# Optimization experiments

Measured on AMD Instinct MI355X. Metric: run time of the kernel, lower is better.

The kernel has to match this reference:

```python
import jax, jax.numpy as jnp
import numpy as np
from jax import lax


def setup_inputs() -> dict:
    key = jax.random.key(0)
    k1, k2, k3, k4 = jax.random.split(key, 4)
    B, C, H, W = 4, 1024, 64, 64
    OUT = 2048
    refer_feat = jax.random.normal(k1, (B, C, H, W), jnp.float32)
    sup_feat = jax.random.normal(k2, (B, C, H, W), jnp.float32)
    # al_conv_one: Conv2d(2048 -> 2, k=3, pad=1); small init keeps offsets in a sane range
    w_off = jax.random.normal(k3, (2, 2 * C, 3, 3), jnp.float32) * 0.01
    b_off = jnp.zeros((2,), jnp.float32)
    # defConv1: DeformConv2d(1024 -> 2048, k=1, bias=False); weight is effectively [O, C]
    w_def = jax.random.normal(k4, (OUT, C), jnp.float32) * (1.0 / np.sqrt(C))
    return {"refer_feat": refer_feat, "sup_feat": sup_feat,
            "w_off": w_off, "b_off": b_off, "w_def": w_def}


def _deform_sample(feat, dy, dx):
    """Bilinear-sample feat[b,:, h+dy, w+dx] with zero padding outside. -> [B,C,H*W]"""
    B, C, H, W = feat.shape
    py = dy + jnp.arange(H, dtype=feat.dtype)[None, :, None]   # [B,H,W]
    px = dx + jnp.arange(W, dtype=feat.dtype)[None, None, :]   # [B,H,W]
    y0 = jnp.floor(py)
    x0 = jnp.floor(px)
    wy1 = py - y0   # frac weights
    wx1 = px - x0
    y0i = y0.astype(jnp.int32)
    x0i = x0.astype(jnp.int32)
    feat_flat = feat.reshape(B, C, H * W)

    def corner(yi, xi, wgt):
        valid = (yi >= 0) & (yi < H) & (xi >= 0) & (xi < W)
        idx = (jnp.clip(yi, 0, H - 1) * W + jnp.clip(xi, 0, W - 1)).reshape(B, 1, H * W)
        g = jnp.take_along_axis(feat_flat, idx, axis=2)          # [B,C,HW]
        return g * (wgt * valid.astype(feat.dtype)).reshape(B, 1, H * W)

    return (corner(y0i, x0i, (1 - wy1) * (1 - wx1))
            + corner(y0i, x0i + 1, (1 - wy1) * wx1)
            + corner(y0i + 1, x0i, wy1 * (1 - wx1))
            + corner(y0i + 1, x0i + 1, wy1 * wx1))


def reference(refer_feat, sup_feat, w_off, b_off, w_def):
    B, C, H, W = sup_feat.shape
    concat_feat = jnp.concatenate([refer_feat, sup_feat], axis=1)      # [B,2C,H,W]
    offset = lax.conv_general_dilated(
        concat_feat, w_off, window_strides=(1, 1), padding='SAME',
        dimension_numbers=('NCHW', 'OIHW', 'NCHW')) + b_off[None, :, None, None]  # [B,2,H,W]
    # torchvision DeformConv2d offset layout for k=1: channel 0 = dy, channel 1 = dx
    sampled = _deform_sample(sup_feat, offset[:, 0], offset[:, 1])     # [B,C,HW]
    out = jnp.einsum('oc,bcl->bol', w_def, sampled)                    # 1x1 conv as GEMM
    return out.reshape(B, w_def.shape[0], H, W)
```

## Files before the change

kernel.cpp:

```cpp
#include <hip/hip_runtime.h>

#define CC   1024
#define C2   2048
#define HH   64
#define WW   64
#define HW   4096
#define MOUT 2048
#define NB   4

typedef short  short8  __attribute__((ext_vector_type(8)));
typedef float  floatx4 __attribute__((ext_vector_type(4)));

static __device__ __forceinline__ unsigned short f2bf(float f) {
  unsigned int u = __builtin_bit_cast(unsigned int, f);
  u = u + 0x7FFFu + ((u >> 16) & 1u);
  return (unsigned short)(u >> 16);
}

static __device__ __forceinline__ void glds16(const unsigned short* g, unsigned short* l) {
  __builtin_amdgcn_global_load_lds(
      (const __attribute__((address_space(1))) void*)g,
      (__attribute__((address_space(3))) void*)l, 16, 0, 0);
}

__global__ __launch_bounds__(256)
void conv_off(const float* __restrict__ refer, const float* __restrict__ sup,
              const float* __restrict__ woff, float* __restrict__ off)
{
  const int cz = blockIdx.x;
  const int ry = blockIdx.y;
  const int b  = blockIdx.z;
  const int wv = threadIdx.x >> 6;
  const int w  = threadIdx.x & 63;
  const int h0 = ry * 8 + wv * 2;

  const int cc0 = cz * 32;
  const float* basep = (cz < 32)
      ? refer + ((size_t)b * CC + cc0) * HW
      : sup   + ((size_t)b * CC + (cc0 - CC)) * HW;

  const int gy0 = h0 - 1;
  const bool top_ok = (gy0 >= 0);
  const bool bot_ok = (h0 + 2 < HH);

  float a00 = 0.f, a01 = 0.f, a10 = 0.f, a11 = 0.f;

  float rn[4];
#pragma unroll
  for (int j = 0; j < 4; j++) {
    const bool ok = (j == 0) ? top_ok : (j == 3) ? bot_ok : true;
    rn[j] = ok ? basep[(gy0 + j) * WW + w] : 0.f;
  }

  for (int ci = 0; ci < 32; ci++) {
    float rc[4];
#pragma unroll
    for (int j = 0; j < 4; j++) rc[j] = rn[j];

    if (ci < 31) {
      const float* pn = basep + (size_t)(ci + 1) * HW;
#pragma unroll
      for (int j = 0; j < 4; j++) {
        const bool ok = (j == 0) ? top_ok : (j == 3) ? bot_ok : true;
        rn[j] = ok ? pn[(gy0 + j) * WW + w] : 0.f;
      }
    }

    float lft[4], rgt[4];
#pragma unroll
    for (int j = 0; j < 4; j++) {
      const float tl = __shfl(rc[j], (w - 1) & 63, 64);
      const float tr = __shfl(rc[j], (w + 1) & 63, 64);
      lft[j] = (w == 0)  ? 0.f : tl;
      rgt[j] = (w == 63) ? 0.f : tr;
    }

    const int cc = cc0 + ci;
    const float* wp0 = woff + (size_t)cc * 9;
    const float* wp1 = woff + (size_t)(C2 + cc) * 9;
#pragma unroll
    for (int ky = 0; ky < 3; ky++) {
      const float w00 = wp0[ky * 3 + 0], w01 = wp0[ky * 3 + 1], w02 = wp0[ky * 3 + 2];
      const float w10 = wp1[ky * 3 + 0], w11 = wp1[ky * 3 + 1], w12 = wp1[ky * 3 + 2];
      a00 += lft[ky]     * w00 + rc[ky]     * w01 + rgt[ky]     * w02;
      a01 += lft[ky]     * w10 + rc[ky]     * w11 + rgt[ky]     * w12;
      a10 += lft[ky + 1] * w00 + rc[ky + 1] * w01 + rgt[ky + 1] * w02;
      a11 += lft[ky + 1] * w10 + rc[ky + 1] * w11 + rgt[ky + 1] * w12;
    }
  }

  atomicAdd(&off[((b * 2 + 0) * HH + h0) * WW + w],     a00);
  atomicAdd(&off[((b * 2 + 1) * HH + h0) * WW + w],     a01);
  atomicAdd(&off[((b * 2 + 0) * HH + h0 + 1) * WW + w], a10);
  atomicAdd(&off[((b * 2 + 1) * HH + h0 + 1) * WW + w], a11);
}

__global__ __launch_bounds__(256)
void cvt_bf16(const float* __restrict__ src, unsigned short* __restrict__ dst, int n4)
{
  const int i = blockIdx.x * 256 + threadIdx.x;
  if (i < n4) {
    const float4 f = ((const float4*)src)[i];
    ushort4 u;
    u.x = f2bf(f.x); u.y = f2bf(f.y); u.z = f2bf(f.z); u.w = f2bf(f.w);
    ((ushort4*)dst)[i] = u;
  }
}

__global__ __launch_bounds__(256)
void sample_kern(const float* __restrict__ sup, const float* __restrict__ off,
                 const float* __restrict__ boff, unsigned short* __restrict__ St)
{
  const int h   = blockIdx.x;
  const int ct  = blockIdx.y;
  const int b   = blockIdx.z;
  const int tid = threadIdx.x;

  __shared__ float swy[64], swx[64];
  __shared__ int   sy0[64], sx0[64];
  __shared__ unsigned short tile[64 * 68];

  if (tid < 64) {
    const float dy = off[((b * 2 + 0) * HH + h) * WW + tid] + boff[0];
    const float dx = off[((b * 2 + 1) * HH + h) * WW + tid] + boff[1];
    const float py = dy + (float)h;
    const float px = dx + (float)tid;
    const float y0f = floorf(py), x0f = floorf(px);
    sy0[tid] = (int)y0f;  sx0[tid] = (int)x0f;
    swy[tid] = py - y0f;  swx[tid] = px - x0f;
  }
  __syncthreads();

  const int l   = tid & 63;
  const int cs0 = tid >> 6;
  const int y0 = sy0[l], x0 = sx0[l];
  const int y1 = y0 + 1, x1 = x0 + 1;
  const float wy1 = swy[l], wx1 = swx[l];
  const float wy0 = 1.f - wy1, wx0 = 1.f - wx1;
  const float vy0 = (y0 >= 0 && y0 < HH) ? 1.f : 0.f;
  const float vy1 = (y1 >= 0 && y1 < HH) ? 1.f : 0.f;
  const float vx0 = (x0 >= 0 && x0 < WW) ? 1.f : 0.f;
  const float vx1 = (x1 >= 0 && x1 < WW) ? 1.f : 0.f;
  const int cy0 = min(max(y0, 0), HH - 1), cy1 = min(max(y1, 0), HH - 1);
  const int cx0 = min(max(x0, 0), WW - 1), cx1 = min(max(x1, 0), WW - 1);
  const int i00 = cy0 * WW + cx0, i01 = cy0 * WW + cx1;
  const int i10 = cy1 * WW + cx0, i11 = cy1 * WW + cx1;
  const float w00 = wy0 * wx0 * vy0 * vx0;
  const float w01 = wy0 * wx1 * vy0 * vx1;
  const float w10 = wy1 * wx0 * vy1 * vx0;
  const float w11 = wy1 * wx1 * vy1 * vx1;

  const int cb = ct * 64;
  for (int cs = cs0; cs < 64; cs += 4) {
    const float* sp = sup + ((size_t)b * CC + cb + cs) * HW;
    const float v = w00 * sp[i00] + w01 * sp[i01] + w10 * sp[i10] + w11 * sp[i11];
    tile[cs * 68 + l] = f2bf(v);
  }
  __syncthreads();
  const int cq  = tid & 15;
  const int ls0 = tid >> 4;
  unsigned short* stb = St + ((size_t)b * HW + h * 64) * CC;
  for (int ls = ls0; ls < 64; ls += 16) {
    ushort4 pk;
    pk.x = tile[(cq * 4 + 0) * 68 + ls];
    pk.y = tile[(cq * 4 + 1) * 68 + ls];
    pk.z = tile[(cq * 4 + 2) * 68 + ls];
    pk.w = tile[(cq * 4 + 3) * 68 + ls];
    *(ushort4*)&stb[(size_t)ls * CC + cb + cq * 4] = pk;
  }
}

__global__ __launch_bounds__(256)
void gemm_bt(const unsigned short* __restrict__ A,
             const unsigned short* __restrict__ Bt,
             float* __restrict__ C)
{
  const int bb = blockIdx.z;
  const int n0 = blockIdx.x * 128;
  const int m0 = blockIdx.y * 128;
  const unsigned short* Bb = Bt + (size_t)bb * HW * CC;
  float* Cb = C + (size_t)bb * (size_t)MOUT * HW;

  __shared__ __align__(16) unsigned short lA[128 * 64];
  __shared__ __align__(16) unsigned short lB[128 * 64];

  const int tid  = threadIdx.x;
  const int wave = tid >> 6;
  const int lane = tid & 63;
  const int wm   = (wave >> 1) * 64;
  const int wn   = (wave & 1) * 64;
  const int lrow = lane & 15;
  const int quad = lane >> 4;

  const int g8 = lane >> 3;
  const int s8 = (lane & 7) ^ g8;
  const unsigned short* gA = A  + (size_t)(m0 + wave * 32 + g8) * CC + s8 * 8;
  const unsigned short* gB = Bb + (size_t)(n0 + wave * 32 + g8) * CC + s8 * 8;

  floatx4 acc[4][4];
#pragma unroll
  for (int i = 0; i < 4; i++)
#pragma unroll
    for (int j = 0; j < 4; j++)
      acc[i][j] = (floatx4){0.f, 0.f, 0.f, 0.f};

  for (int k0 = 0; k0 < CC; k0 += 64) {
    __syncthreads();
#pragma unroll
    for (int q = 0; q < 4; q++) {
      glds16(gA + (size_t)q * 8 * CC + k0, &lA[(wave * 32 + q * 8) * 64]);
      glds16(gB + (size_t)q * 8 * CC + k0, &lB[(wave * 32 + q * 8) * 64]);
    }
    __syncthreads();

#pragma unroll
    for (int ks = 0; ks < 2; ks++) {
      short8 af[4], bfr[4];
#pragma unroll
      for (int t = 0; t < 4; t++) {
        const int sw = ((ks * 4 + quad) ^ (lrow & 7)) * 8;
        af[t]  = *(const short8*)&lA[(wm + t * 16 + lrow) * 64 + sw];
        bfr[t] = *(const short8*)&lB[(wn + t * 16 + lrow) * 64 + sw];
      }
#pragma unroll
      for (int i = 0; i < 4; i++)
#pragma unroll
        for (int j = 0; j < 4; j++)
          acc[i][j] = __builtin_amdgcn_mfma_f32_16x16x32_bf16(af[i], bfr[j], acc[i][j], 0, 0, 0);
    }
  }

#pragma unroll
  for (int i = 0; i < 4; i++) {
    const int mbase = m0 + wm + i * 16 + quad * 4;
#pragma unroll
    for (int j = 0; j < 4; j++) {
      const int n = n0 + wn + j * 16 + lrow;
      float* cp = Cb + (size_t)mbase * HW + n;
#pragma unroll
      for (int r = 0; r < 4; r++)
        cp[(size_t)r * HW] = acc[i][j][r];
    }
  }
}

extern "C" void kernel_launch(void* const* d_in, const int* in_sizes, int n_in,
                              void* d_out, int out_size, void* d_ws, size_t ws_size,
                              hipStream_t stream)
{
  const float* refer = (const float*)d_in[0];
  const float* sup   = (const float*)d_in[1];
  const float* woff  = (const float*)d_in[2];
  const float* boff  = (const float*)d_in[3];
  const float* wdef  = (const float*)d_in[4];
  float* out = (float*)d_out;

  char* ws = (char*)d_ws;
  float* off            = (float*)ws;
  unsigned short* wdefb = (unsigned short*)(ws + (512u << 10));
  unsigned short* St    = (unsigned short*)(ws + (512u << 10) + (4u << 20));

  hipMemsetAsync(off, 0, (size_t)NB * 2 * HW * sizeof(float), stream);
  conv_off<<<dim3(64, 8, NB), 256, 0, stream>>>(refer, sup, woff, off);
  cvt_bf16<<<dim3((MOUT * CC / 4 + 255) / 256), 256, 0, stream>>>(wdef, wdefb, MOUT * CC / 4);
  sample_kern<<<dim3(HH, 16, NB), 256, 0, stream>>>(sup, off, boff, St);
  gemm_bt<<<dim3(HW / 128, MOUT / 128, NB), 256, 0, stream>>>(wdefb, St, out);
}
```

Before: 381.0 us.

## Rewrite GEMM with 256x256 tiles and triple-buffered async LDS pipeline

Replaces the 128x128 single-buffered bf16 MFMA GEMM with a 256x256 tile kernel using 512 threads. It adds a three-stage LDS ring that issues global-to-LDS loads two K-steps ahead, overlapping loads with MFMA work. It also splits each K-step into two MFMA half-phases with barriers and s_setprio. The larger tile aims to raise arithmetic intensity and hide memory latency, at the cost of more registers, more LDS and fewer blocks (512 total).

After: 387.7 us. No clear change (+1.8%).

```diff
diff --git a/kernel.cpp b/kernel.cpp
--- a/kernel.cpp
+++ b/kernel.cpp
@@ -170,72 +170,112 @@
   }
 }
 
-__global__ __launch_bounds__(256)
-void gemm_bt(const unsigned short* __restrict__ A,
-             const unsigned short* __restrict__ Bt,
-             float* __restrict__ C)
+#define STAGE_A(s, kk) do { \
+  glds16(gA + (kk),                    &lA[s][(wave * 16) * 32]); \
+  glds16(gA + (size_t)128 * CC + (kk), &lA[s][(128 + wave * 16) * 32]); \
+} while (0)
+#define STAGE_B(s, kk) do { \
+  glds16(gB + (kk),                    &lB[s][(wave * 16) * 32]); \
+  glds16(gB + (size_t)128 * CC + (kk), &lB[s][(128 + wave * 16) * 32]); \
+} while (0)
+
+__global__ __launch_bounds__(512, 2)
+void gemm_bt256(const unsigned short* __restrict__ A,
+                const unsigned short* __restrict__ Bt,
+                float* __restrict__ C)
 {
   const int bb = blockIdx.z;
-  const int n0 = blockIdx.x * 128;
-  const int m0 = blockIdx.y * 128;
+  const int n0 = blockIdx.x * 256;
+  const int m0 = blockIdx.y * 256;
   const unsigned short* Bb = Bt + (size_t)bb * HW * CC;
   float* Cb = C + (size_t)bb * (size_t)MOUT * HW;
 
-  __shared__ __align__(16) unsigned short lA[128 * 64];
-  __shared__ __align__(16) unsigned short lB[128 * 64];
+  __shared__ __align__(16) unsigned short lA[3][256 * 32];
+  __shared__ __align__(16) unsigned short lB[3][256 * 32];
 
   const int tid  = threadIdx.x;
   const int wave = tid >> 6;
   const int lane = tid & 63;
-  const int wm   = (wave >> 1) * 64;
-  const int wn   = (wave & 1) * 64;
+  const int wmA  = (wave >> 2) * 128;
+  const int wnB  = (wave & 3) * 64;
   const int lrow = lane & 15;
   const int quad = lane >> 4;
-
-  const int g8 = lane >> 3;
-  const int s8 = (lane & 7) ^ g8;
-  const unsigned short* gA = A  + (size_t)(m0 + wave * 32 + g8) * CC + s8 * 8;
-  const unsigned short* gB = Bb + (size_t)(n0 + wave * 32 + g8) * CC + s8 * 8;
-
-  floatx4 acc[4][4];
-#pragma unroll
-  for (int i = 0; i < 4; i++)
+  const int rdo  = ((quad ^ ((lrow >> 1) & 3)) << 3);
+
+  const int srow = tid >> 2;
+  const int schk = (tid & 3) ^ ((tid >> 3) & 3);
+  const unsigned short* gA = A  + (size_t)(m0 + srow) * CC + schk * 8;
+  const unsigned short* gB = Bb + (size_t)(n0 + srow) * CC + schk * 8;
+
+  STAGE_A(0, 0);  STAGE_B(0, 0);
+  STAGE_A(1, 32); STAGE_B(1, 32);
+
+  floatx4 acc[8][4];
+#pragma unroll
+  for (int i = 0; i < 8; i++)
 #pragma unroll
     for (int j = 0; j < 4; j++)
       acc[i][j] = (floatx4){0.f, 0.f, 0.f, 0.f};
 
-  for (int k0 = 0; k0 < CC; k0 += 64) {
-    __syncthreads();
-#pragma unroll
-    for (int q = 0; q < 4; q++) {
-      glds16(gA + (size_t)q * 8 * CC + k0, &lA[(wave * 32 + q * 8) * 64]);
-      glds16(gB + (size_t)q * 8 * CC + k0, &lB[(wave * 32 + q * 8) * 64]);
-    }
-    __syncthreads();
-
-#pragma unroll
-    for (int ks = 0; ks < 2; ks++) {
-      short8 af[4], bfr[4];
-#pragma unroll
-      for (int t = 0; t < 4; t++) {
-        const int sw = ((ks * 4 + quad) ^ (lrow & 7)) * 8;
-        af[t]  = *(const short8*)&lA[(wm + t * 16 + lrow) * 64 + sw];
-        bfr[t] = *(const short8*)&lB[(wn + t * 16 + lrow) * 64 + sw];
-      }
-#pragma unroll
-      for (int i = 0; i < 4; i++)
-#pragma unroll
-        for (int j = 0; j < 4; j++)
-          acc[i][j] = __builtin_amdgcn_mfma_f32_16x16x32_bf16(af[i], bfr[j], acc[i][j], 0, 0, 0);
-    }
-  }
-
-#pragma unroll
-  for (int i = 0; i < 4; i++) {
-    const int mbase = m0 + wm + i * 16 + quad * 4;
+  asm volatile("s_waitcnt vmcnt(4)" ::: "memory");
+  __builtin_amdgcn_s_barrier();
+  asm volatile("" ::: "memory");
+
+  auto tile_step = [&](int t, int cb, int sb, bool st, int vm) {
+    const int k2 = (t + 2) * 32;
+
+    short8 af[4], bfr[4];
+#pragma unroll
+    for (int i = 0; i < 4; i++)
+      af[i] = *(const short8*)&lA[cb][(wmA + i * 16 + lrow) * 32 + rdo];
+#pragma unroll
+    for (int j = 0; j < 4; j++)
+      bfr[j] = *(const short8*)&lB[cb][(wnB + j * 16 + lrow) * 32 + rdo];
+    if (st) STAGE_A(sb, k2);
+    __builtin_amdgcn_s_barrier();
+    __builtin_amdgcn_s_setprio(1);
+#pragma unroll
+    for (int i = 0; i < 4; i++)
+#pragma unroll
+      for (int j = 0; j < 4; j++)
+        acc[i][j] = __builtin_amdgcn_mfma_f32_16x16x32_bf16(af[i], bfr[j], acc[i][j], 0, 0, 0);
+    __builtin_amdgcn_s_setprio(0);
+    __builtin_amdgcn_s_barrier();
+
+    short8 ag[4];
+#pragma unroll
+    for (int i = 0; i < 4; i++)
+      ag[i] = *(const short8*)&lA[cb][(wmA + 64 + i * 16 + lrow) * 32 + rdo];
+    if (st) STAGE_B(sb, k2);
+    __builtin_amdgcn_s_barrier();
+    __builtin_amdgcn_s_setprio(1);
+#pragma unroll
+    for (int i = 0; i < 4; i++)
+#pragma unroll
+      for (int j = 0; j < 4; j++)
+        acc[4 + i][j] = __builtin_amdgcn_mfma_f32_16x16x32_bf16(ag[i], bfr[j], acc[4 + i][j], 0, 0, 0);
+    __builtin_amdgcn_s_setprio(0);
+    if (vm == 4)      asm volatile("s_waitcnt vmcnt(4)" ::: "memory");
+    else if (vm == 0) asm volatile("s_waitcnt vmcnt(0)" ::: "memory");
+    __builtin_amdgcn_s_barrier();
+    asm volatile("" ::: "memory");
+  };
+
+#pragma unroll 1
+  for (int tt = 0; tt < 30; tt += 3) {
+    tile_step(tt + 0, 0, 2, true, 4);
+    tile_step(tt + 1, 1, 0, true, 4);
+    tile_step(tt + 2, 2, 1, true, 4);
+  }
+  tile_step(30, 0, 2, false, 0);
+  tile_step(31, 1, 0, false, -1);
+
+#pragma unroll
+  for (int i = 0; i < 8; i++) {
+    const int mbase = m0 + wmA + i * 16 + quad * 4;
 #pragma unroll
     for (int j = 0; j < 4; j++) {
-      const int n = n0 + wn + j * 16 + lrow;
+      const int n = n0 + wnB + j * 16 + lrow;
       float* cp = Cb + (size_t)mbase * HW + n;
 #pragma unroll
       for (int r = 0; r < 4; r++)
@@ -264,5 +304,5 @@
   conv_off<<<dim3(64, 8, NB), 256, 0, stream>>>(refer, sup, woff, off);
   cvt_bf16<<<dim3((MOUT * CC / 4 + 255) / 256), 256, 0, stream>>>(wdef, wdefb, MOUT * CC / 4);
   sample_kern<<<dim3(HH, 16, NB), 256, 0, stream>>>(sup, off, boff, St);
-  gemm_bt<<<dim3(HW / 128, MOUT / 128, NB), 256, 0, stream>>>(wdefb, St, out);
-}
+  gemm_bt256<<<dim3(HW / 256, MOUT / 256, NB), 512, 0, stream>>>(wdefb, St, out);
+}
```

## Pipeline GEMM with triple-buffered async LDS loads and 128x256 tiles

Applied to the files above, without the earlier changes.

Replaces the single-buffered, double-barrier GEMM loop with a three-stage LDS ring. Direct global-to-LDS loads for tile t+2 are issued while MFMAs run on tile t, and vmcnt waits with one barrier per step keep them in order. The block tile grows to 128x256 with a K step of 32, each wave computes 64x128, and a remapped tile order is meant to improve L2 reuse. Launch bounds now request two blocks per CU, and s_setprio is raised around the MFMA bursts. The aim is to hide global load latency and cut barrier stalls, at the cost of more accumulator registers and LDS per block, which could limit occupancy.

Result: slower. 392.7 us (+3.1%).

```diff
diff --git a/kernel.cpp b/kernel.cpp
--- a/kernel.cpp
+++ b/kernel.cpp
@@ -170,72 +170,96 @@
   }
 }
 
-__global__ __launch_bounds__(256)
-void gemm_bt(const unsigned short* __restrict__ A,
-             const unsigned short* __restrict__ Bt,
-             float* __restrict__ C)
-{
-  const int bb = blockIdx.z;
-  const int n0 = blockIdx.x * 128;
-  const int m0 = blockIdx.y * 128;
+#define STAGE_A(s, kk) do { \
+  glds16(gA + (kk),                   &lA[s][(wave * 16) * 32]); \
+  glds16(gA + (size_t)64 * CC + (kk), &lA[s][(64 + wave * 16) * 32]); \
+} while (0)
+#define STAGE_B(s, kk) do { \
+  glds16(gB + (kk),                    &lB[s][(wave * 16) * 32]); \
+  glds16(gB + (size_t)64 * CC + (kk),  &lB[s][(64  + wave * 16) * 32]); \
+  glds16(gB + (size_t)128 * CC + (kk), &lB[s][(128 + wave * 16) * 32]); \
+  glds16(gB + (size_t)192 * CC + (kk), &lB[s][(192 + wave * 16) * 32]); \
+} while (0)
+
+#define TILE(T, CB, SB, ST, VM) do { \
+  short8 af[4], bq[8]; \
+  _Pragma("unroll") \
+  for (int i_ = 0; i_ < 4; i_++) \
+    af[i_] = *(const short8*)&lA[CB][(wmA + i_ * 16 + lrow) * 32 + rdo]; \
+  _Pragma("unroll") \
+  for (int j_ = 0; j_ < 8; j_++) \
+    bq[j_] = *(const short8*)&lB[CB][(wnB + j_ * 16 + lrow) * 32 + rdo]; \
+  if (ST) { const int k2_ = ((T) + 2) * 32; STAGE_A(SB, k2_); STAGE_B(SB, k2_); } \
+  __builtin_amdgcn_s_setprio(1); \
+  _Pragma("unroll") \
+  for (int i_ = 0; i_ < 4; i_++) \
+    _Pragma("unroll") \
+    for (int j_ = 0; j_ < 8; j_++) \
+      acc[i_][j_] = __builtin_amdgcn_mfma_f32_16x16x32_bf16(af[i_], bq[j_], acc[i_][j_], 0, 0, 0); \
+  __builtin_amdgcn_s_setprio(0); \
+  if ((VM) == 6)      asm volatile("s_waitcnt vmcnt(6)" ::: "memory"); \
+  else if ((VM) == 0) asm volatile("s_waitcnt vmcnt(0)" ::: "memory"); \
+  if ((VM) != 99) __builtin_amdgcn_s_barrier(); \
+} while (0)
+
+__global__ __launch_bounds__(256, 2)
+void gemm_bt128(const unsigned short* __restrict__ A,
+                const unsigned short* __restrict__ Bt,
+                float* __restrict__ C)
+{
+  const int slot = blockIdx.x + (blockIdx.y << 4) + (blockIdx.z << 8);
+  const int tile = ((slot & 7) << 7) + (slot >> 3);
+  const int m0 = (tile & 15) * 128;
+  const int n0 = ((tile >> 4) & 15) * 256;
+  const int bb = tile >> 8;
   const unsigned short* Bb = Bt + (size_t)bb * HW * CC;
   float* Cb = C + (size_t)bb * (size_t)MOUT * HW;
 
-  __shared__ __align__(16) unsigned short lA[128 * 64];
-  __shared__ __align__(16) unsigned short lB[128 * 64];
+  __shared__ __align__(16) unsigned short lA[3][128 * 32];
+  __shared__ __align__(16) unsigned short lB[3][256 * 32];
 
   const int tid  = threadIdx.x;
   const int wave = tid >> 6;
   const int lane = tid & 63;
-  const int wm   = (wave >> 1) * 64;
-  const int wn   = (wave & 1) * 64;
+  const int wmA  = (wave >> 1) * 64;
+  const int wnB  = (wave & 1) * 128;
   const int lrow = lane & 15;
   const int quad = lane >> 4;
-
-  const int g8 = lane >> 3;
-  const int s8 = (lane & 7) ^ g8;
-  const unsigned short* gA = A  + (size_t)(m0 + wave * 32 + g8) * CC + s8 * 8;
-  const unsigned short* gB = Bb + (size_t)(n0 + wave * 32 + g8) * CC + s8 * 8;
-
-  floatx4 acc[4][4];
+  const int rdo  = ((quad ^ ((lrow >> 1) & 3)) << 3);
+
+  const int srow = tid >> 2;
+  const int schk = (tid & 3) ^ ((tid >> 3) & 3);
+  const unsigned short* gA = A  + (size_t)(m0 + srow) * CC + schk * 8;
+  const unsigned short* gB = Bb + (size_t)(n0 + srow) * CC + schk * 8;
+
+  STAGE_A(0, 0);  STAGE_B(0, 0);
+  STAGE_A(1, 32); STAGE_B(1, 32);
+
+  floatx4 acc[4][8];
 #pragma unroll
   for (int i = 0; i < 4; i++)
 #pragma unroll
-    for (int j = 0; j < 4; j++)
+    for (int j = 0; j < 8; j++)
       acc[i][j] = (floatx4){0.f, 0.f, 0.f, 0.f};
 
-  for (int k0 = 0; k0 < CC; k0 += 64) {
-    __syncthreads();
-#pragma unroll
-    for (int q = 0; q < 4; q++) {
-      glds16(gA + (size_t)q * 8 * CC + k0, &lA[(wave * 32 + q * 8) * 64]);
-      glds16(gB + (size_t)q * 8 * CC + k0, &lB[(wave * 32 + q * 8) * 64]);
-    }
-    __syncthreads();
-
-#pragma unroll
-    for (int ks = 0; ks < 2; ks++) {
-      short8 af[4], bfr[4];
-#pragma unroll
-      for (int t = 0; t < 4; t++) {
-        const int sw = ((ks * 4 + quad) ^ (lrow & 7)) * 8;
-        af[t]  = *(const short8*)&lA[(wm + t * 16 + lrow) * 64 + sw];
-        bfr[t] = *(const short8*)&lB[(wn + t * 16 + lrow) * 64 + sw];
-      }
-#pragma unroll
-      for (int i = 0; i < 4; i++)
-#pragma unroll
-        for (int j = 0; j < 4; j++)
-          acc[i][j] = __builtin_amdgcn_mfma_f32_16x16x32_bf16(af[i], bfr[j], acc[i][j], 0, 0, 0);
-    }
-  }
+  asm volatile("s_waitcnt vmcnt(6)" ::: "memory");
+  __builtin_amdgcn_s_barrier();
+
+#pragma unroll 1
+  for (int t = 0; t < 30; t += 3) {
+    TILE(t + 0, 0, 2, 1, 6);
+    TILE(t + 1, 1, 0, 1, 6);
+    TILE(t + 2, 2, 1, 1, 6);
+  }
+  TILE(30, 0, 0, 0, 0);
+  TILE(31, 1, 0, 0, 99);
 
 #pragma unroll
   for (int i = 0; i < 4; i++) {
-    const int mbase = m0 + wm + i * 16 + quad * 4;
-#pragma unroll
-    for (int j = 0; j < 4; j++) {
-      const int n = n0 + wn + j * 16 + lrow;
+    const int mbase = m0 + wmA + i * 16 + quad * 4;
+#pragma unroll
+    for (int j = 0; j < 8; j++) {
+      const int n = n0 + wnB + j * 16 + lrow;
       float* cp = Cb + (size_t)mbase * HW + n;
 #pragma unroll
       for (int r = 0; r < 4; r++)
@@ -264,5 +288,5 @@
   conv_off<<<dim3(64, 8, NB), 256, 0, stream>>>(refer, sup, woff, off);
   cvt_bf16<<<dim3((MOUT * CC / 4 + 255) / 256), 256, 0, stream>>>(wdef, wdefb, MOUT * CC / 4);
   sample_kern<<<dim3(HH, 16, NB), 256, 0, stream>>>(sup, off, boff, St);
-  gemm_bt<<<dim3(HW / 128, MOUT / 128, NB), 256, 0, stream>>>(wdefb, St, out);
-}
+  gemm_bt128<<<dim3(HW / 256, MOUT / 128, NB), 256, 0, stream>>>(wdefb, St, out);
+}
```
